# Performance work log

Measured on AMD Instinct MI355X. Metric: run time of the kernel, lower is better.

## Reference

```python
import jax, jax.numpy as jnp
import numpy as np

N_NODES = 100000


def gcn_layer(x, src, dst, ew, W, b, n_nodes):
    # PyG GCNConv: h = x @ W, symmetric norm with self-loops (weight 1), scatter-add, + bias
    h = x @ W  # [N, D_out]
    # degree includes self-loop weight 1
    deg = jax.ops.segment_sum(ew, dst, num_segments=n_nodes) + 1.0  # [N]
    dinv = jnp.where(deg > 0, jax.lax.rsqrt(deg), 0.0)  # [N]
    norm = dinv[src] * ew * dinv[dst]  # [E]
    msgs = norm[:, None] * h[src]  # [E, D_out] gathered + scaled messages
    agg = jax.ops.segment_sum(msgs, dst, num_segments=n_nodes)  # scatter-add at dst
    # self-loop contribution: norm_ii = dinv[i]^2
    return agg + (dinv * dinv)[:, None] * h + b


def setup_inputs() -> dict:
    key = jax.random.key(0)
    k1, k2, k3, k4, k5, k6 = jax.random.split(key, 6)
    n, e = N_NODES, 1600000
    d_in, d_hid, d_out = 128, 48, 32
    x = jax.random.normal(k1, (n, d_in), dtype=jnp.float32)
    edge_index = jax.random.randint(k2, (2, e), 0, n, dtype=jnp.int64)
    edge_weight = jax.random.uniform(k3, (e,), dtype=jnp.float32)
    s1 = 1.0 / np.sqrt(d_in)
    s2 = 1.0 / np.sqrt(d_hid)
    W1 = jax.random.uniform(k4, (d_in, d_hid), dtype=jnp.float32, minval=-s1, maxval=s1)
    b1 = jnp.zeros((d_hid,), dtype=jnp.float32)
    W2 = jax.random.uniform(k5, (d_hid, d_out), dtype=jnp.float32, minval=-s2, maxval=s2)
    b2 = jnp.zeros((d_out,), dtype=jnp.float32)
    return {"x": x, "edge_index": edge_index, "edge_weight": edge_weight,
            "W1": W1, "b1": b1, "W2": W2, "b2": b2}


def reference(x, edge_index, edge_weight, W1, b1, W2, b2):
    src, dst = edge_index[0], edge_index[1]
    n = x.shape[0]
    h = gcn_layer(x, src, dst, edge_weight, W1, b1, n)
    h = jax.nn.relu(h)  # dropout is identity in eval mode
    out = gcn_layer(h, src, dst, edge_weight, W2, b2, n)
    return out
```

## Files before the change

kernel.cpp:

```cpp
#include <hip/hip_runtime.h>


#define DIN1 128
#define DHID 48
#define DOUT 32

typedef _Float16 half4_t __attribute__((ext_vector_type(4)));


__global__ __launch_bounds__(256) void bin_count(const int* __restrict__ dst,
                                                 int* __restrict__ bcnt, int E) {
    __shared__ int h[256];
    const int tid = threadIdx.x;
    h[tid] = 0;
    __syncthreads();
    const int base = blockIdx.x * 2048;
#pragma unroll
    for (int j = 0; j < 8; ++j) {
        int e = base + j * 256 + tid;
        if (e < E) atomicAdd(&h[dst[e] >> 9], 1);
    }
    __syncthreads();
    if (h[tid]) atomicAdd(&bcnt[tid], h[tid]);
}

__global__ __launch_bounds__(256) void bucket_scan(const int* __restrict__ bcnt,
                                                   int* __restrict__ bbase,
                                                   int* __restrict__ cursor, int E, int nb) {
    __shared__ int s[256];
    const int tid = threadIdx.x;
    int v = (tid < nb) ? bcnt[tid] : 0;
    s[tid] = v;
    __syncthreads();
    for (int off = 1; off < 256; off <<= 1) {
        int t = (tid >= off) ? s[tid - off] : 0;
        __syncthreads();
        s[tid] += t;
        __syncthreads();
    }
    int excl = s[tid] - v;
    bbase[tid] = excl;
    cursor[tid] = excl;
    if (tid == nb - 1) bbase[nb] = s[tid];
}

__global__ __launch_bounds__(256) void bin_scatter(const int* __restrict__ src,
                                                   const int* __restrict__ dst,
                                                   const float* __restrict__ ew,
                                                   int* __restrict__ cursor,
                                                   int2* __restrict__ mid, int E) {
    __shared__ int lcnt[256], loff[256], gbase[256], s[256];
    __shared__ int2 stage[2048];
    __shared__ unsigned char sbk[2048];
    const int tid = threadIdx.x;
    const int base = blockIdx.x * 2048;
    const int cnt = min(2048, E - base);
    lcnt[tid] = 0;
    __syncthreads();
    int myb[8], myr[8];
    int2 mye[8];
#pragma unroll
    for (int j = 0; j < 8; ++j) {
        int e = base + j * 256 + tid;
        myb[j] = -1;
        if (e < E) {
            int d = dst[e];
            int b = d >> 9;
            mye[j] = make_int2(src[e] | ((d & 511) << 17), __float_as_int(ew[e]));
            myr[j] = atomicAdd(&lcnt[b], 1);
            myb[j] = b;
        }
    }
    __syncthreads();
    s[tid] = lcnt[tid];
    __syncthreads();
    for (int off = 1; off < 256; off <<= 1) {
        int t = (tid >= off) ? s[tid - off] : 0;
        __syncthreads();
        s[tid] += t;
        __syncthreads();
    }
    loff[tid] = s[tid] - lcnt[tid];
    if (lcnt[tid] > 0) gbase[tid] = atomicAdd(&cursor[tid], lcnt[tid]);
    __syncthreads();
#pragma unroll
    for (int j = 0; j < 8; ++j) {
        if (myb[j] >= 0) {
            int pos = loff[myb[j]] + myr[j];
            stage[pos] = mye[j];
            sbk[pos] = (unsigned char)myb[j];
        }
    }
    __syncthreads();
    for (int i = tid; i < cnt; i += 256) {
        int b = sbk[i];
        mid[gbase[b] + (i - loff[b])] = stage[i];
    }
}

__global__ __launch_bounds__(256) void bucket_build(const int2* __restrict__ mid,
                                                    const int* __restrict__ bbase,
                                                    int2* __restrict__ ep,
                                                    float* __restrict__ dinvg,
                                                    int* __restrict__ row_start,
                                                    int* __restrict__ countg, int n) {
    __shared__ float sdeg[512];
    __shared__ int scnt[512], soff[512], scur[512], s2[256];
    const int tid = threadIdx.x;
    const int b = blockIdx.x;
    const int n0 = b << 9;
    const int nr = min(512, n - n0);
    const int e0 = bbase[b], e1 = bbase[b + 1];
    for (int i = tid; i < 512; i += 256) { sdeg[i] = 0.0f; scnt[i] = 0; }
    __syncthreads();
    for (int i = e0 + tid; i < e1; i += 256) {
        int2 p = mid[i];
        int dl = (p.x >> 17) & 511;
        atomicAdd(&scnt[dl], 1);
        atomicAdd(&sdeg[dl], __int_as_float(p.y));
    }
    __syncthreads();
    int a0 = scnt[2 * tid], a1 = scnt[2 * tid + 1];
    s2[tid] = a0 + a1;
    __syncthreads();
    for (int off = 1; off < 256; off <<= 1) {
        int t = (tid >= off) ? s2[tid - off] : 0;
        __syncthreads();
        s2[tid] += t;
        __syncthreads();
    }
    int excl = s2[tid] - (a0 + a1);
    soff[2 * tid] = excl;
    soff[2 * tid + 1] = excl + a0;
    scur[2 * tid] = excl;
    scur[2 * tid + 1] = excl + a0;
    __syncthreads();
    for (int i = tid; i < nr; i += 256) {
        dinvg[n0 + i] = rsqrtf(sdeg[i] + 1.0f);
        row_start[n0 + i] = e0 + soff[i];
        countg[n0 + i] = scnt[i];
    }
    __syncthreads();
    for (int i = e0 + tid; i < e1; i += 256) {
        int2 p = mid[i];
        int dl = (p.x >> 17) & 511;
        int r = atomicAdd(&scur[dl], 1);
        ep[e0 + r] = make_int2(p.x & 0x1FFFF, p.y);
    }
}


template <int DIN_, int DOUT_, bool RELU_IN>
__global__ __launch_bounds__(256, 4) void gemm_kernel(const float* __restrict__ X,
                                                      const float* __restrict__ W,
                                                      _Float16* __restrict__ H, int n) {
    constexpr int ROWS = 32;
    constexpr int CPT = DOUT_ / 16;
    constexpr int P4 = DIN_ / 4 + 1;
    __shared__ float sX[ROWS * P4 * 4];
    __shared__ float sWt[DOUT_ * P4 * 4];
    const int tid = threadIdx.x;
    const int row0 = blockIdx.x * ROWS;

    const float4* W4 = reinterpret_cast<const float4*>(W);
    for (int i = tid; i < DIN_ * DOUT_ / 4; i += 256) {
        float4 v = W4[i];
        int k = (4 * i) / DOUT_;
        int c = (4 * i) % DOUT_;
        sWt[(c + 0) * P4 * 4 + k] = v.x;
        sWt[(c + 1) * P4 * 4 + k] = v.y;
        sWt[(c + 2) * P4 * 4 + k] = v.z;
        sWt[(c + 3) * P4 * 4 + k] = v.w;
    }
    const float4* X4 = reinterpret_cast<const float4*>(X);
    constexpr int C4 = DIN_ / 4;
    for (int i = tid; i < ROWS * C4; i += 256) {
        int r = i / C4;
        int k4 = i % C4;
        float4 v = make_float4(0.f, 0.f, 0.f, 0.f);
        if (row0 + r < n) v = X4[(size_t)(row0 + r) * C4 + k4];
        if (RELU_IN) {
            v.x = fmaxf(v.x, 0.f); v.y = fmaxf(v.y, 0.f);
            v.z = fmaxf(v.z, 0.f); v.w = fmaxf(v.w, 0.f);
        }
        reinterpret_cast<float4*>(sX)[r * P4 + k4] = v;
    }
    __syncthreads();

    const int cg = tid & 15;
    const int r0 = (tid >> 4) * 2;
    const float4* sX4 = reinterpret_cast<const float4*>(sX);
    const float4* sWt4 = reinterpret_cast<const float4*>(sWt);
    float acc[2][CPT];
#pragma unroll
    for (int ri = 0; ri < 2; ++ri)
#pragma unroll
        for (int j = 0; j < CPT; ++j) acc[ri][j] = 0.0f;

#pragma unroll 4
    for (int k4 = 0; k4 < C4; ++k4) {
        float4 xa0 = sX4[(r0 + 0) * P4 + k4];
        float4 xa1 = sX4[(r0 + 1) * P4 + k4];
#pragma unroll
        for (int j = 0; j < CPT; ++j) {
            float4 wb = sWt4[(cg + j * 16) * P4 + k4];
            acc[0][j] = fmaf(xa0.x, wb.x, acc[0][j]);
            acc[0][j] = fmaf(xa0.y, wb.y, acc[0][j]);
            acc[0][j] = fmaf(xa0.z, wb.z, acc[0][j]);
            acc[0][j] = fmaf(xa0.w, wb.w, acc[0][j]);
            acc[1][j] = fmaf(xa1.x, wb.x, acc[1][j]);
            acc[1][j] = fmaf(xa1.y, wb.y, acc[1][j]);
            acc[1][j] = fmaf(xa1.z, wb.z, acc[1][j]);
            acc[1][j] = fmaf(xa1.w, wb.w, acc[1][j]);
        }
    }
#pragma unroll
    for (int ri = 0; ri < 2; ++ri) {
        int r = row0 + r0 + ri;
        if (r < n) {
#pragma unroll
            for (int j = 0; j < CPT; ++j)
                H[(size_t)r * DOUT_ + cg + j * 16] = (_Float16)acc[ri][j];
        }
    }
}

template <int D>
__global__ __launch_bounds__(256) void aggregate_kernel(const int* __restrict__ row_start,
                                                        const int* __restrict__ count,
                                                        const int2* __restrict__ ep,
                                                        const _Float16* __restrict__ h,
                                                        const float* __restrict__ dinv,
                                                        const float* __restrict__ b,
                                                        float* __restrict__ out, int n) {
    constexpr int C = D / 4;
    int gid = blockIdx.x * blockDim.x + threadIdx.x;
    if (gid >= n * C) return;
    int i = gid / C;
    int c = gid % C;
    const half4_t* h4 = reinterpret_cast<const half4_t*>(h);
    float di = dinv[i];
    float sl = di * di;
    half4_t hs = h4[(size_t)i * C + c];
    float4 acc;
    acc.x = sl * (float)hs[0];
    acc.y = sl * (float)hs[1];
    acc.z = sl * (float)hs[2];
    acc.w = sl * (float)hs[3];
    int r0 = row_start[i], r1 = r0 + count[i];
    for (int k = r0; k < r1; ++k) {
        int2 p = ep[k];
        float nm = dinv[p.x] * __int_as_float(p.y) * di;
        half4_t hv = h4[(size_t)p.x * C + c];
        acc.x = fmaf(nm, (float)hv[0], acc.x);
        acc.y = fmaf(nm, (float)hv[1], acc.y);
        acc.z = fmaf(nm, (float)hv[2], acc.z);
        acc.w = fmaf(nm, (float)hv[3], acc.w);
    }
    float4 bv = reinterpret_cast<const float4*>(b)[c];
    acc.x += bv.x; acc.y += bv.y; acc.z += bv.z; acc.w += bv.w;
    reinterpret_cast<float4*>(out)[(size_t)i * C + c] = acc;
}

extern "C" void kernel_launch(void* const* d_in, const int* in_sizes, int n_in,
                              void* d_out, int out_size, void* d_ws, size_t ws_size,
                              hipStream_t stream) {
    const float* x  = (const float*)d_in[0];
    const int*   ei = (const int*)d_in[1];
    const float* ew = (const float*)d_in[2];
    const float* W1 = (const float*)d_in[3];
    const float* b1 = (const float*)d_in[4];
    const float* W2 = (const float*)d_in[5];
    const float* b2 = (const float*)d_in[6];
    float* out = (float*)d_out;

    const int n = in_sizes[0] / DIN1;
    const int E = in_sizes[1] / 2;
    const int* src = ei;
    const int* dst = ei + E;
    const int nb = (n + 511) >> 9;

    char* w = (char*)d_ws;
    int*   bcnt      = (int*)w;   w += 256 * 4;
    int*   bbase     = (int*)w;   w += 272 * 4;
    int*   cursor    = (int*)w;   w += 256 * 4;
    float* dinv      = (float*)w; w += (size_t)n * 4;
    int*   row_start = (int*)w;   w += (size_t)n * 4;
    int*   count     = (int*)w;   w += (size_t)n * 4;
    int2*  mid       = (int2*)w;  w += (size_t)E * 8;
    int2*  ep        = (int2*)w;  w += (size_t)E * 8;
    _Float16* h1     = (_Float16*)w; w += (size_t)n * DHID * 2;
    float* out1      = (float*)w; w += (size_t)n * DHID * 4;
    _Float16* h2     = (_Float16*)w;

    const int eblk = (E + 2047) / 2048;

    hipMemsetAsync(bcnt, 0, 256 * 4, stream);
    bin_count<<<eblk, 256, 0, stream>>>(dst, bcnt, E);
    bucket_scan<<<1, 256, 0, stream>>>(bcnt, bbase, cursor, E, nb);
    bin_scatter<<<eblk, 256, 0, stream>>>(src, dst, ew, cursor, mid, E);
    bucket_build<<<nb, 256, 0, stream>>>(mid, bbase, ep, dinv, row_start, count, n);

    gemm_kernel<DIN1, DHID, false><<<(n + 31) / 32, 256, 0, stream>>>(x, W1, h1, n);
    aggregate_kernel<DHID><<<(n * (DHID / 4) + 255) / 256, 256, 0, stream>>>(
        row_start, count, ep, h1, dinv, b1, out1, n);

    gemm_kernel<DHID, DOUT, true><<<(n + 31) / 32, 256, 0, stream>>>(out1, W2, h2, n);
    aggregate_kernel<DOUT><<<(n * (DOUT / 4) + 255) / 256, 256, 0, stream>>>(
        row_start, count, ep, h2, dinv, b2, out, n);
}
```

Measured before the change: 320.6 us.

## Fuse bucket scan into scatter, co-launch scatter with first GEMM, degree-sort rows

Removes the standalone bucket_scan kernel: each scatter block and each bucket_build block recomputes the bucket prefix sum from bcnt, and a zeroed cursor0 supplies per-bucket offsets. The edge scatter and the first GEMM run in one launch, with blocks split by index, so the two independent stages can overlap. bucket_build also sorts nodes within each 512-node bucket by in-degree and writes an ord permutation, which aggregation uses so that neighbouring threads handle rows of similar length and warp divergence drops. The cost is redundant scan work in every block, an extra indirection in aggregation, and a fused kernel whose dynamic LDS is sized for the GEMM.

```diff
diff --git a/kernel.cpp b/kernel.cpp
--- a/kernel.cpp
+++ b/kernel.cpp
@@ -24,38 +24,33 @@
     if (h[tid]) atomicAdd(&bcnt[tid], h[tid]);
 }
 
-__global__ __launch_bounds__(256) void bucket_scan(const int* __restrict__ bcnt,
-                                                   int* __restrict__ bbase,
-                                                   int* __restrict__ cursor, int E, int nb) {
-    __shared__ int s[256];
+struct ScatterSmem {
+    int lcnt[256], loff[256], gbase[256], s[256], bb[256];
+    int2 stage[2048];
+    unsigned char sbk[2048];
+};
+
+__device__ __forceinline__ void scatter_body(char* smem, const int* __restrict__ src,
+                                             const int* __restrict__ dst,
+                                             const float* __restrict__ ew,
+                                             const int* __restrict__ bcnt,
+                                             int* __restrict__ cursor0,
+                                             int2* __restrict__ mid, int E, int blk) {
+    ScatterSmem& sm = *reinterpret_cast<ScatterSmem*>(smem);
     const int tid = threadIdx.x;
-    int v = (tid < nb) ? bcnt[tid] : 0;
-    s[tid] = v;
+    const int base = blk * 2048;
+    const int cnt = min(2048, E - base);
+    int bv = bcnt[tid];
+    sm.s[tid] = bv;
+    sm.lcnt[tid] = 0;
     __syncthreads();
     for (int off = 1; off < 256; off <<= 1) {
-        int t = (tid >= off) ? s[tid - off] : 0;
-        __syncthreads();
-        s[tid] += t;
-        __syncthreads();
-    }
-    int excl = s[tid] - v;
-    bbase[tid] = excl;
-    cursor[tid] = excl;
-    if (tid == nb - 1) bbase[nb] = s[tid];
-}
-
-__global__ __launch_bounds__(256) void bin_scatter(const int* __restrict__ src,
-                                                   const int* __restrict__ dst,
-                                                   const float* __restrict__ ew,
-                                                   int* __restrict__ cursor,
-                                                   int2* __restrict__ mid, int E) {
-    __shared__ int lcnt[256], loff[256], gbase[256], s[256];
-    __shared__ int2 stage[2048];
-    __shared__ unsigned char sbk[2048];
-    const int tid = threadIdx.x;
-    const int base = blockIdx.x * 2048;
-    const int cnt = min(2048, E - base);
-    lcnt[tid] = 0;
+        int t = (tid >= off) ? sm.s[tid - off] : 0;
+        __syncthreads();
+        sm.s[tid] += t;
+        __syncthreads();
+    }
+    sm.bb[tid] = sm.s[tid] - bv;
     __syncthreads();
     int myb[8], myr[8];
     int2 mye[8];
@@ -67,100 +62,48 @@
             int d = dst[e];
             int b = d >> 9;
             mye[j] = make_int2(src[e] | ((d & 511) << 17), __float_as_int(ew[e]));
-            myr[j] = atomicAdd(&lcnt[b], 1);
+            myr[j] = atomicAdd(&sm.lcnt[b], 1);
             myb[j] = b;
         }
     }
     __syncthreads();
-    s[tid] = lcnt[tid];
+    sm.s[tid] = sm.lcnt[tid];
     __syncthreads();
     for (int off = 1; off < 256; off <<= 1) {
-        int t = (tid >= off) ? s[tid - off] : 0;
-        __syncthreads();
-        s[tid] += t;
-        __syncthreads();
-    }
-    loff[tid] = s[tid] - lcnt[tid];
-    if (lcnt[tid] > 0) gbase[tid] = atomicAdd(&cursor[tid], lcnt[tid]);
+        int t = (tid >= off) ? sm.s[tid - off] : 0;
+        __syncthreads();
+        sm.s[tid] += t;
+        __syncthreads();
+    }
+    sm.loff[tid] = sm.s[tid] - sm.lcnt[tid];
+    if (sm.lcnt[tid] > 0)
+        sm.gbase[tid] = sm.bb[tid] + atomicAdd(&cursor0[tid], sm.lcnt[tid]);
     __syncthreads();
 #pragma unroll
     for (int j = 0; j < 8; ++j) {
         if (myb[j] >= 0) {
-            int pos = loff[myb[j]] + myr[j];
-            stage[pos] = mye[j];
-            sbk[pos] = (unsigned char)myb[j];
+            int pos = sm.loff[myb[j]] + myr[j];
+            sm.stage[pos] = mye[j];
+            sm.sbk[pos] = (unsigned char)myb[j];
         }
     }
     __syncthreads();
     for (int i = tid; i < cnt; i += 256) {
-        int b = sbk[i];
-        mid[gbase[b] + (i - loff[b])] = stage[i];
-    }
-}
-
-__global__ __launch_bounds__(256) void bucket_build(const int2* __restrict__ mid,
-                                                    const int* __restrict__ bbase,
-                                                    int2* __restrict__ ep,
-                                                    float* __restrict__ dinvg,
-                                                    int* __restrict__ row_start,
-                                                    int* __restrict__ countg, int n) {
-    __shared__ float sdeg[512];
-    __shared__ int scnt[512], soff[512], scur[512], s2[256];
-    const int tid = threadIdx.x;
-    const int b = blockIdx.x;
-    const int n0 = b << 9;
-    const int nr = min(512, n - n0);
-    const int e0 = bbase[b], e1 = bbase[b + 1];
-    for (int i = tid; i < 512; i += 256) { sdeg[i] = 0.0f; scnt[i] = 0; }
-    __syncthreads();
-    for (int i = e0 + tid; i < e1; i += 256) {
-        int2 p = mid[i];
-        int dl = (p.x >> 17) & 511;
-        atomicAdd(&scnt[dl], 1);
-        atomicAdd(&sdeg[dl], __int_as_float(p.y));
-    }
-    __syncthreads();
-    int a0 = scnt[2 * tid], a1 = scnt[2 * tid + 1];
-    s2[tid] = a0 + a1;
-    __syncthreads();
-    for (int off = 1; off < 256; off <<= 1) {
-        int t = (tid >= off) ? s2[tid - off] : 0;
-        __syncthreads();
-        s2[tid] += t;
-        __syncthreads();
-    }
-    int excl = s2[tid] - (a0 + a1);
-    soff[2 * tid] = excl;
-    soff[2 * tid + 1] = excl + a0;
-    scur[2 * tid] = excl;
-    scur[2 * tid + 1] = excl + a0;
-    __syncthreads();
-    for (int i = tid; i < nr; i += 256) {
-        dinvg[n0 + i] = rsqrtf(sdeg[i] + 1.0f);
-        row_start[n0 + i] = e0 + soff[i];
-        countg[n0 + i] = scnt[i];
-    }
-    __syncthreads();
-    for (int i = e0 + tid; i < e1; i += 256) {
-        int2 p = mid[i];
-        int dl = (p.x >> 17) & 511;
-        int r = atomicAdd(&scur[dl], 1);
-        ep[e0 + r] = make_int2(p.x & 0x1FFFF, p.y);
-    }
-}
-
+        int b = sm.sbk[i];
+        mid[sm.gbase[b] + (i - sm.loff[b])] = sm.stage[i];
+    }
+}
 
 template <int DIN_, int DOUT_, bool RELU_IN>
-__global__ __launch_bounds__(256, 4) void gemm_kernel(const float* __restrict__ X,
-                                                      const float* __restrict__ W,
-                                                      _Float16* __restrict__ H, int n) {
+__device__ __forceinline__ void gemm_body(char* smem, const float* __restrict__ X,
+                                          const float* __restrict__ W,
+                                          _Float16* __restrict__ H, int n, int row0) {
     constexpr int ROWS = 32;
     constexpr int CPT = DOUT_ / 16;
     constexpr int P4 = DIN_ / 4 + 1;
-    __shared__ float sX[ROWS * P4 * 4];
-    __shared__ float sWt[DOUT_ * P4 * 4];
+    float* sX = reinterpret_cast<float*>(smem);
+    float* sWt = sX + ROWS * P4 * 4;
     const int tid = threadIdx.x;
-    const int row0 = blockIdx.x * ROWS;
 
     const float4* W4 = reinterpret_cast<const float4*>(W);
     for (int i = tid; i < DIN_ * DOUT_ / 4; i += 256) {
@@ -225,9 +168,106 @@
     }
 }
 
+__global__ __launch_bounds__(256, 4) void scatter_gemm1(
+    const int* __restrict__ src, const int* __restrict__ dst, const float* __restrict__ ew,
+    const int* __restrict__ bcnt, int* __restrict__ cursor0, int2* __restrict__ mid,
+    int E, int nsb, const float* __restrict__ X, const float* __restrict__ W,
+    _Float16* __restrict__ H, int n) {
+    extern __shared__ char smem[];
+    if ((int)blockIdx.x < nsb)
+        scatter_body(smem, src, dst, ew, bcnt, cursor0, mid, E, blockIdx.x);
+    else
+        gemm_body<DIN1, DHID, false>(smem, X, W, H, n, (blockIdx.x - nsb) * 32);
+}
+
+template <int DIN_, int DOUT_, bool RELU_IN>
+__global__ __launch_bounds__(256, 4) void gemm_kernel(const float* __restrict__ X,
+                                                      const float* __restrict__ W,
+                                                      _Float16* __restrict__ H, int n) {
+    constexpr int P4 = DIN_ / 4 + 1;
+    __shared__ char smem[(32 * P4 * 4 + DOUT_ * P4 * 4) * 4];
+    gemm_body<DIN_, DOUT_, RELU_IN>(smem, X, W, H, n, blockIdx.x * 32);
+}
+
+__global__ __launch_bounds__(256) void bucket_build(const int2* __restrict__ mid,
+                                                    const int* __restrict__ bcnt,
+                                                    int2* __restrict__ ep,
+                                                    float* __restrict__ dinvg,
+                                                    int* __restrict__ row_start,
+                                                    int* __restrict__ countg,
+                                                    int* __restrict__ ordg, int n) {
+    __shared__ float sdeg[512];
+    __shared__ int scnt[512], soff[512], scur[512], s2[256];
+    __shared__ int dh[64], dcur[64], dbase[64];
+    __shared__ int sE0, sE1;
+    const int tid = threadIdx.x;
+    const int b = blockIdx.x;
+    const int n0 = b << 9;
+    const int nr = min(512, n - n0);
+    int bv = bcnt[tid];
+    s2[tid] = bv;
+    __syncthreads();
+    for (int off = 1; off < 256; off <<= 1) {
+        int t = (tid >= off) ? s2[tid - off] : 0;
+        __syncthreads();
+        s2[tid] += t;
+        __syncthreads();
+    }
+    if (tid == b) { sE1 = s2[tid]; sE0 = s2[tid] - bv; }
+    for (int i = tid; i < 512; i += 256) { sdeg[i] = 0.0f; scnt[i] = 0; }
+    if (tid < 64) { dh[tid] = 0; dcur[tid] = 0; }
+    __syncthreads();
+    const int e0 = sE0, e1 = sE1;
+    for (int i = e0 + tid; i < e1; i += 256) {
+        int2 p = mid[i];
+        int dl = (p.x >> 17) & 511;
+        atomicAdd(&scnt[dl], 1);
+        atomicAdd(&sdeg[dl], __int_as_float(p.y));
+    }
+    __syncthreads();
+    int a0 = scnt[2 * tid], a1 = scnt[2 * tid + 1];
+    s2[tid] = a0 + a1;
+    __syncthreads();
+    for (int off = 1; off < 256; off <<= 1) {
+        int t = (tid >= off) ? s2[tid - off] : 0;
+        __syncthreads();
+        s2[tid] += t;
+        __syncthreads();
+    }
+    int excl = s2[tid] - (a0 + a1);
+    soff[2 * tid] = excl;
+    soff[2 * tid + 1] = excl + a0;
+    scur[2 * tid] = excl;
+    scur[2 * tid + 1] = excl + a0;
+    __syncthreads();
+    for (int i = tid; i < nr; i += 256) atomicAdd(&dh[min(scnt[i], 63)], 1);
+    __syncthreads();
+    if (tid == 0) {
+        int run = 0;
+        for (int d = 0; d < 64; ++d) { dbase[d] = run; run += dh[d]; }
+    }
+    __syncthreads();
+    for (int i = tid; i < nr; i += 256) {
+        int d = min(scnt[i], 63);
+        int r = dbase[d] + atomicAdd(&dcur[d], 1);
+        row_start[n0 + r] = e0 + soff[i];
+        countg[n0 + r] = scnt[i];
+        ordg[n0 + r] = n0 + i;
+        dinvg[n0 + i] = rsqrtf(sdeg[i] + 1.0f);
+    }
+    __syncthreads();
+    for (int i = e0 + tid; i < e1; i += 256) {
+        int2 p = mid[i];
+        int dl = (p.x >> 17) & 511;
+        int r = atomicAdd(&scur[dl], 1);
+        ep[e0 + r] = make_int2(p.x & 0x1FFFF, p.y);
+    }
+}
+
 template <int D>
 __global__ __launch_bounds__(256) void aggregate_kernel(const int* __restrict__ row_start,
                                                         const int* __restrict__ count,
+                                                        const int* __restrict__ ord,
                                                         const int2* __restrict__ ep,
                                                         const _Float16* __restrict__ h,
                                                         const float* __restrict__ dinv,
@@ -236,18 +276,19 @@
     constexpr int C = D / 4;
     int gid = blockIdx.x * blockDim.x + threadIdx.x;
     if (gid >= n * C) return;
-    int i = gid / C;
+    int ir = gid / C;
     int c = gid % C;
+    int orig = ord[ir];
     const half4_t* h4 = reinterpret_cast<const half4_t*>(h);
-    float di = dinv[i];
+    float di = dinv[orig];
     float sl = di * di;
-    half4_t hs = h4[(size_t)i * C + c];
+    half4_t hs = h4[(size_t)orig * C + c];
     float4 acc;
     acc.x = sl * (float)hs[0];
     acc.y = sl * (float)hs[1];
     acc.z = sl * (float)hs[2];
     acc.w = sl * (float)hs[3];
-    int r0 = row_start[i], r1 = r0 + count[i];
+    int r0 = row_start[ir], r1 = r0 + count[ir];
     for (int k = r0; k < r1; ++k) {
         int2 p = ep[k];
         float nm = dinv[p.x] * __int_as_float(p.y) * di;
@@ -259,7 +300,7 @@
     }
     float4 bv = reinterpret_cast<const float4*>(b)[c];
     acc.x += bv.x; acc.y += bv.y; acc.z += bv.z; acc.w += bv.w;
-    reinterpret_cast<float4*>(out)[(size_t)i * C + c] = acc;
+    reinterpret_cast<float4*>(out)[(size_t)orig * C + c] = acc;
 }
 
 extern "C" void kernel_launch(void* const* d_in, const int* in_sizes, int n_in,
@@ -282,11 +323,11 @@
 
     char* w = (char*)d_ws;
     int*   bcnt      = (int*)w;   w += 256 * 4;
-    int*   bbase     = (int*)w;   w += 272 * 4;
-    int*   cursor    = (int*)w;   w += 256 * 4;
+    int*   cursor0   = (int*)w;   w += 256 * 4;
     float* dinv      = (float*)w; w += (size_t)n * 4;
     int*   row_start = (int*)w;   w += (size_t)n * 4;
     int*   count     = (int*)w;   w += (size_t)n * 4;
+    int*   ord       = (int*)w;   w += (size_t)n * 4;
     int2*  mid       = (int2*)w;  w += (size_t)E * 8;
     int2*  ep        = (int2*)w;  w += (size_t)E * 8;
     _Float16* h1     = (_Float16*)w; w += (size_t)n * DHID * 2;
@@ -294,18 +335,19 @@
     _Float16* h2     = (_Float16*)w;
 
     const int eblk = (E + 2047) / 2048;
-
-    hipMemsetAsync(bcnt, 0, 256 * 4, stream);
+    const int gblk = (n + 31) / 32;
+    const size_t fused_lds = (32 * (DIN1 / 4 + 1) * 4 + DHID * (DIN1 / 4 + 1) * 4) * 4;
+
+    hipMemsetAsync(bcnt, 0, 512 * 4, stream);
     bin_count<<<eblk, 256, 0, stream>>>(dst, bcnt, E);
-    bucket_scan<<<1, 256, 0, stream>>>(bcnt, bbase, cursor, E, nb);
-    bin_scatter<<<eblk, 256, 0, stream>>>(src, dst, ew, cursor, mid, E);
-    bucket_build<<<nb, 256, 0, stream>>>(mid, bbase, ep, dinv, row_start, count, n);
-
-    gemm_kernel<DIN1, DHID, false><<<(n + 31) / 32, 256, 0, stream>>>(x, W1, h1, n);
+    scatter_gemm1<<<eblk + gblk, 256, fused_lds, stream>>>(src, dst, ew, bcnt, cursor0, mid,
+                                                           E, eblk, x, W1, h1, n);
+    bucket_build<<<nb, 256, 0, stream>>>(mid, bcnt, ep, dinv, row_start, count, ord, n);
+
     aggregate_kernel<DHID><<<(n * (DHID / 4) + 255) / 256, 256, 0, stream>>>(
-        row_start, count, ep, h1, dinv, b1, out1, n);
-
-    gemm_kernel<DHID, DOUT, true><<<(n + 31) / 32, 256, 0, stream>>>(out1, W2, h2, n);
+        row_start, count, ord, ep, h1, dinv, b1, out1, n);
+
+    gemm_kernel<DHID, DOUT, true><<<gblk, 256, 0, stream>>>(out1, W2, h2, n);
     aggregate_kernel<DOUT><<<(n * (DOUT / 4) + 255) / 256, 256, 0, stream>>>(
-        row_start, count, ep, h2, dinv, b2, out, n);
-}
+        row_start, count, ord, ep, h2, dinv, b2, out, n);
+}
```

Measured after the change: 319.7 us. Within noise of the previous version (-0.3%).
